# Optimization experiments

Hardware: AMD Instinct MI355X
Metric: run time of the kernel (lower is better)

The kernel has to match this reference:

```python
import jax, jax.numpy as jnp
import numpy as np
from jax import lax

HEADS = 8
LN_EPS = 1e-5


def setup_inputs() -> dict:
    key = jax.random.key(0)
    k = jax.random.split(key, 8)
    B, C, H, W, r = 4, 64, 64, 64, 4
    T = H * W
    x = jax.random.normal(k[0], (B, C, H, W), dtype=jnp.float32)
    conv_w = jax.random.normal(k[1], (C, C, r, r), dtype=jnp.float32) * 0.02  # OIHW
    conv_b = jnp.zeros((C,), dtype=jnp.float32)
    ln_g = jnp.ones((C,), dtype=jnp.float32)
    ln_b = jnp.zeros((C,), dtype=jnp.float32)
    Wqkv = jax.random.normal(k[2], (C, 3 * C), dtype=jnp.float32) * 0.02  # to_qvk (no bias)
    W0 = jax.random.normal(k[3], (C, C), dtype=jnp.float32) * 0.02  # output proj (no bias)
    E = jax.random.normal(k[4], (T, T // 4), dtype=jnp.float32)  # Linformer proj (randn in torch fwd)
    return {"x": x, "conv_w": conv_w, "conv_b": conv_b, "ln_g": ln_g,
            "ln_b": ln_b, "Wqkv": Wqkv, "W0": W0, "E": E}


def _layernorm2d(y, g, b):
    # LayerNorm over channel dim of NCHW (torch: permute to NHWC, LN last dim)
    yt = y.transpose(0, 2, 3, 1)  # b h w c
    mu = yt.mean(-1, keepdims=True)
    var = ((yt - mu) ** 2).mean(-1, keepdims=True)
    yt = (yt - mu) * lax.rsqrt(var + LN_EPS) * g + b
    return yt.transpose(0, 3, 1, 2)


def reference(x, conv_w, conv_b, ln_g, ln_b, Wqkv, W0, E):
    B, C, H, W = x.shape
    T = H * W
    dh = C // HEADS
    r = conv_w.shape[-1]

    # reducer: conv(stride=r) + LayerNorm2d. NOTE: faithful to the torch module,
    # this result is computed but NEVER used by the output (dead code in source).
    red = lax.conv_general_dilated(x, conv_w, (r, r), 'VALID',
                                   dimension_numbers=('NCHW', 'OIHW', 'NCHW'))
    red = red + conv_b[None, :, None, None]
    _red = _layernorm2d(red, ln_g, ln_b)  # unused, matches source

    # tokens from full-resolution x: b c h w -> b (h w) c
    xf = x.reshape(B, C, T).transpose(0, 2, 1)  # [B,T,C]
    qkv = xf @ Wqkv  # [B,T,3C]
    # rearrange 'b t (d k h)' with k=3, h=HEADS -> composite order (d, k, h)
    qkv = qkv.reshape(B, T, dh, 3, HEADS)
    q = qkv[:, :, :, 0, :].transpose(0, 3, 1, 2)  # [B,h,T,d]
    kk = qkv[:, :, :, 1, :].transpose(0, 3, 1, 2)
    v = qkv[:, :, :, 2, :].transpose(0, 3, 1, 2)

    # Linformer low-rank projection of V and K: [B,h,T,d] x [T,k] -> [B,h,k,d]
    v = jnp.einsum('bhjd,jk->bhkd', v, E)
    kk = jnp.einsum('bhjd,jk->bhkd', kk, E)

    scale = dh ** -0.5
    scores = jnp.einsum('bhid,bhjd->bhij', q, kk) * scale  # [B,h,T,k]
    attn = jax.nn.softmax(scores, axis=-1)
    out = jnp.einsum('bhij,bhjd->bhid', attn, v)  # [B,h,T,d]

    out = out.transpose(0, 2, 1, 3).reshape(B, T, C)  # b h i d -> b i (h d)
    out = out @ W0  # [B,T,C]
    return out.transpose(0, 2, 1).reshape(B, C, H, W)
```

## Files before the change

### kernel.cpp

```cpp
#include <hip/hip_runtime.h>

#define T_DIM 4096
#define KD    1024
#define SCALE2 (0.35355339059327373f * 1.4426950408889634f)
#define XS_PITCH 264
#define XP_PITCH 17
#define WK_PITCH 136
#define VC_H 648

extern "C" __device__ float __ocml_native_exp2_f32(float);

typedef __attribute__((ext_vector_type(8))) short bf16x8;
typedef __attribute__((ext_vector_type(4))) float f32x4;
typedef __attribute__((ext_vector_type(16))) float f32x16;

__device__ inline unsigned short f2bf(float f) {
  unsigned u = __float_as_uint(f);
  unsigned r = u + 0x7fffu + ((u >> 16) & 1u);
  return (unsigned short)(r >> 16);
}

__device__ inline unsigned cvt_pk_bf16(float a, float b) {
  unsigned ua = __float_as_uint(a); ua += 0x7fffu + ((ua >> 16) & 1u);
  unsigned ub = __float_as_uint(b); ub += 0x7fffu + ((ub >> 16) & 1u);
  return (ua >> 16) | (ub & 0xffff0000u);
}

__device__ inline bf16x8 mk8(unsigned a, unsigned b, unsigned c, unsigned d) {
  union { unsigned u[4]; bf16x8 v; } x;
  x.u[0] = a; x.u[1] = b; x.u[2] = c; x.u[3] = d; return x.v;
}

__global__ __launch_bounds__(512) void k_front(const float* __restrict__ x,
                                               const float* __restrict__ E,
                                               const float* __restrict__ Wqkv,
                                               uint2* __restrict__ Kg,
                                               unsigned short* __restrict__ Vg,
                                               float* __restrict__ Q) {
  __shared__ __attribute__((aligned(16))) float SMEM[8 * 64 * XP_PITCH];
  __shared__ __attribute__((aligned(16))) float Wkvs[64 * WK_PITCH];
  unsigned short* xs = (unsigned short*)SMEM;
  float* XPs = SMEM;

  const int bid = blockIdx.x;
  const int tid = threadIdx.x;

  if (bid < 256) {
    const int kb = (bid & 7) + 8 * (bid >> 5);
    const int b  = (bid >> 3) & 3;
    const int k0 = kb * 16;
    const int lane = tid & 63, w = tid >> 6;
    const int li = lane & 15, lg = lane >> 4;

#pragma unroll
    for (int i = 0; i < 16; ++i) {
      const int idx = tid + i * 512;
      const int c = idx >> 7, j = idx & 127;
      const int cg = j >> 3, d = j & 7;
      const int sel = (cg < 8) ? 1 : 2, h = cg & 7;
      Wkvs[c * WK_PITCH + j] = Wqkv[c * 192 + sel * 8 + h + d * 24];
    }

    f32x4 acc[4] = {};
    const int tl  = (tid & 127) * 2;
    const int chp = tid >> 7;
    const int tloc = w * 32 + lg * 8;

    for (int ct = 0; ct < 16; ++ct) {
      const float* xb = x + ((size_t)b * 64 + chp) * T_DIM + ct * 256 + tl;
#pragma unroll 4
      for (int it = 0; it < 16; ++it) {
        const int c = it * 4 + chp;
        float2 v = *(const float2*)(xb + (size_t)(it * 4) * T_DIM);
        *(unsigned*)(&xs[c * XS_PITCH + tl]) = cvt_pk_bf16(v.x, v.y);
      }
      __syncthreads();

      const int tb = ct * 256 + tloc;
      float bv[8];
#pragma unroll
      for (int j = 0; j < 8; ++j)
        bv[j] = E[(size_t)(tb + j) * KD + k0 + li];
      bf16x8 bq = mk8(cvt_pk_bf16(bv[0], bv[1]), cvt_pk_bf16(bv[2], bv[3]),
                      cvt_pk_bf16(bv[4], bv[5]), cvt_pk_bf16(bv[6], bv[7]));
#pragma unroll
      for (int mt = 0; mt < 4; ++mt) {
        bf16x8 af8 = *(const bf16x8*)(&xs[(mt * 16 + li) * XS_PITCH + tloc]);
        acc[mt] = __builtin_amdgcn_mfma_f32_16x16x32_bf16(af8, bq, acc[mt], 0, 0, 0);
      }
      __syncthreads();
    }

#pragma unroll
    for (int mt = 0; mt < 4; ++mt)
#pragma unroll
      for (int r = 0; r < 4; ++r)
        XPs[(w * 64 + mt * 16 + lg * 4 + r) * XP_PITCH + li] = acc[mt][r];
    __syncthreads();

#pragma unroll
    for (int i = 0; i < 2; ++i) {
      const int idx = tid + i * 512;
      const int c = idx >> 4, k = idx & 15;
      float s = 0.f;
#pragma unroll
      for (int wp = 0; wp < 8; ++wp) s += XPs[(wp * 64 + c) * XP_PITCH + k];
      XPs[c * XP_PITCH + k] = s;
    }
    __syncthreads();

    {
      const int k  = tid & 15;
      const int cg = (tid >> 4) & 15;
      const int dh = tid >> 8;
      float a4[4] = {0.f, 0.f, 0.f, 0.f};
#pragma unroll 8
      for (int c = 0; c < 64; ++c) {
        const float xv = XPs[c * XP_PITCH + k];
        const float4 wv = *(const float4*)(&Wkvs[c * WK_PITCH + cg * 8 + dh * 4]);
        a4[0] += xv * wv.x; a4[1] += xv * wv.y;
        a4[2] += xv * wv.z; a4[3] += xv * wv.w;
      }
      const int h = cg & 7, bh = b * 8 + h, kk2 = k0 + k;
      if (cg < 8) {
        Kg[(size_t)bh * 2048 + kk2 * 2 + dh] =
            make_uint2(cvt_pk_bf16(a4[0] * SCALE2, a4[1] * SCALE2),
                       cvt_pk_bf16(a4[2] * SCALE2, a4[3] * SCALE2));
      } else {
#pragma unroll
        for (int d = 0; d < 4; ++d)
          Vg[(size_t)(bh * 8 + dh * 4 + d) * KD + kk2] = f2bf(a4[d]);
      }
    }
  } else {
    const int idx = bid - 256;
    const int g  = idx & 7;
    const int tt = (idx >> 3) & 7;
    const int b  = idx >> 6;
    const int t  = tt * 512 + tid;
    const int col0 = g * 24;

    float acc[8];
#pragma unroll
    for (int j = 0; j < 8; ++j) acc[j] = 0.f;
    const float* xb = x + (size_t)b * 64 * T_DIM + t;
#pragma unroll 4
    for (int c = 0; c < 64; ++c) {
      float xv = xb[(size_t)c * T_DIM];
      const float* wr = Wqkv + c * 192 + col0;
#pragma unroll
      for (int h = 0; h < 8; ++h) acc[h] += xv * wr[h];
    }
#pragma unroll
    for (int h = 0; h < 8; ++h)
      Q[(((size_t)(b * 8 + h)) * 8 + g) * T_DIM + t] = acc[h];
  }
}

__global__ __launch_bounds__(512, 4) void k_attn(const float* __restrict__ Q,
                                                 const uint2* __restrict__ Kg,
                                                 const unsigned short* __restrict__ Vg,
                                                 const float* __restrict__ W0,
                                                 float* __restrict__ out) {
  __shared__ __attribute__((aligned(16))) unsigned short Kc[2][8 * 64 * 8];
  __shared__ __attribute__((aligned(16))) unsigned short Vc[2][8 * VC_H];
  __shared__ __attribute__((aligned(16))) float W0s[64 * 64];

  const int iy = blockIdx.x;
  const int b  = blockIdx.y;
  const int tid = threadIdx.x;
  const int w = tid >> 6;
  const int lane = tid & 63;
  const int icol = lane & 31, half = lane >> 5;
  const int i0 = iy * 32;
  const int bh = b * 8 + w;

#pragma unroll
  for (int i = 0; i < 8; ++i) W0s[tid + i * 512] = W0[tid + i * 512];

  {
    const int bu = tid >> 8, h = (tid >> 5) & 7, j2 = tid & 31;
    *(unsigned*)(&Vc[bu][h * VC_H + 8 * 72 + j2 * 2]) = 0x3F803F80u;
  }

  bf16x8 qf8 = {};
  if (lane < 32) {
    const float* qp = Q + (size_t)bh * 8 * T_DIM + i0 + icol;
    float q0 = qp[0],          q1 = qp[T_DIM],     q2 = qp[2 * T_DIM];
    float q3 = qp[3 * T_DIM],  q4 = qp[4 * T_DIM], q5 = qp[5 * T_DIM];
    float q6 = qp[6 * T_DIM],  q7 = qp[7 * T_DIM];
    qf8 = mk8(cvt_pk_bf16(q0, q1), cvt_pk_bf16(q2, q3),
              cvt_pk_bf16(q4, q5), cvt_pk_bf16(q6, q7));
  }

  const uint4* kg4    = (const uint4*)Kg + (size_t)b * 8192;
  const unsigned* vg2 = (const unsigned*)Vg + (size_t)b * 32768;

  {
    const int h = tid >> 6, j = tid & 63;
    *(uint4*)(&Kc[0][(h * 64 + j) * 8]) = kg4[h * 1024 + j];
#pragma unroll
    for (int i = 0; i < 4; ++i) {
      const int idx = tid + i * 512;
      const int hh = idx >> 8, d = (idx >> 5) & 7, j2 = idx & 31;
      *(unsigned*)(&Vc[0][hh * VC_H + d * 72 + j2 * 2]) = vg2[(hh * 8 + d) * 512 + j2];
    }
  }
  __syncthreads();

  f32x16 accO = {};
  int buf = 0;
  for (int jc = 0; jc < 16; ++jc) {
    uint4 kreg = {}; unsigned vreg[4] = {};
    if (jc < 15) {
      const int h = tid >> 6, j = tid & 63;
      kreg = kg4[h * 1024 + (jc + 1) * 64 + j];
#pragma unroll
      for (int i = 0; i < 4; ++i) {
        const int idx = tid + i * 512;
        const int hh = idx >> 8, d = (idx >> 5) & 7, j2 = idx & 31;
        vreg[i] = vg2[(hh * 8 + d) * 512 + (jc + 1) * 32 + j2];
      }
    }

#pragma unroll
    for (int sub = 0; sub < 2; ++sub) {
      const int jl = sub * 32;
      bf16x8 kf8 = {};
      if (lane < 32) kf8 = *(const bf16x8*)(&Kc[buf][(w * 64 + jl + lane) * 8]);
      f32x16 z = {};
      __builtin_amdgcn_s_setprio(1);
      f32x16 st = __builtin_amdgcn_mfma_f32_32x32x16_bf16(kf8, qf8, z, 0, 0, 0);
      __builtin_amdgcn_s_setprio(0);

      unsigned e0, e1, e2, e3, e4, e5, e6, e7;
      {
        float p0  = __ocml_native_exp2_f32(st[0]),  p1  = __ocml_native_exp2_f32(st[1]);
        float p2  = __ocml_native_exp2_f32(st[2]),  p3  = __ocml_native_exp2_f32(st[3]);
        float p4  = __ocml_native_exp2_f32(st[4]),  p5  = __ocml_native_exp2_f32(st[5]);
        float p6  = __ocml_native_exp2_f32(st[6]),  p7  = __ocml_native_exp2_f32(st[7]);
        float p8  = __ocml_native_exp2_f32(st[8]),  p9  = __ocml_native_exp2_f32(st[9]);
        float p10 = __ocml_native_exp2_f32(st[10]), p11 = __ocml_native_exp2_f32(st[11]);
        float p12 = __ocml_native_exp2_f32(st[12]), p13 = __ocml_native_exp2_f32(st[13]);
        float p14 = __ocml_native_exp2_f32(st[14]), p15 = __ocml_native_exp2_f32(st[15]);
        asm("v_cvt_pk_bf16_f32 %0, %1, %2" : "=v"(e0) : "v"(p0),  "v"(p1));
        asm("v_cvt_pk_bf16_f32 %0, %1, %2" : "=v"(e1) : "v"(p2),  "v"(p3));
        asm("v_cvt_pk_bf16_f32 %0, %1, %2" : "=v"(e2) : "v"(p4),  "v"(p5));
        asm("v_cvt_pk_bf16_f32 %0, %1, %2" : "=v"(e3) : "v"(p6),  "v"(p7));
        asm("v_cvt_pk_bf16_f32 %0, %1, %2" : "=v"(e4) : "v"(p8),  "v"(p9));
        asm("v_cvt_pk_bf16_f32 %0, %1, %2" : "=v"(e5) : "v"(p10), "v"(p11));
        asm("v_cvt_pk_bf16_f32 %0, %1, %2" : "=v"(e6) : "v"(p12), "v"(p13));
        asm("v_cvt_pk_bf16_f32 %0, %1, %2" : "=v"(e7) : "v"(p14), "v"(p15));
      }
      asm("v_permlane32_swap_b32 %0, %1" : "+v"(e0), "+v"(e2));
      asm("v_permlane32_swap_b32 %0, %1" : "+v"(e1), "+v"(e3));
      asm("v_permlane32_swap_b32 %0, %1" : "+v"(e4), "+v"(e6));
      asm("v_permlane32_swap_b32 %0, %1" : "+v"(e5), "+v"(e7));

      bf16x8 va0 = {}, va1 = {};
      if (icol < 9) {
        const unsigned short* vp = &Vc[buf][w * VC_H + icol * 72 + jl + half * 8];
        va0 = *(const bf16x8*)(vp);
        va1 = *(const bf16x8*)(vp + 16);
      }
      __builtin_amdgcn_s_setprio(1);
      accO = __builtin_amdgcn_mfma_f32_32x32x16_bf16(va0, mk8(e0, e1, e2, e3), accO, 0, 0, 0);
      accO = __builtin_amdgcn_mfma_f32_32x32x16_bf16(va1, mk8(e4, e5, e6, e7), accO, 0, 0, 0);
      __builtin_amdgcn_s_setprio(0);
    }

    if (jc < 15) {
      const int h = tid >> 6, j = tid & 63;
      *(uint4*)(&Kc[buf ^ 1][(h * 64 + j) * 8]) = kreg;
#pragma unroll
      for (int i = 0; i < 4; ++i) {
        const int idx = tid + i * 512;
        const int hh = idx >> 8, d = (idx >> 5) & 7, j2 = idx & 31;
        *(unsigned*)(&Vc[buf ^ 1][hh * VC_H + d * 72 + j2 * 2]) = vreg[i];
      }
    }
    __syncthreads();
    buf ^= 1;
  }

  float* Os = (float*)Kc;
  {
    float inv = 1.0f / __shfl(accO[4], icol);
    if (lane < 32 || half) {
      float4 o = make_float4(accO[0] * inv, accO[1] * inv,
                             accO[2] * inv, accO[3] * inv);
      *(float2*)(&Os[icol * 66 + w * 8 + half * 4])     = make_float2(o.x, o.y);
      *(float2*)(&Os[icol * 66 + w * 8 + half * 4 + 2]) = make_float2(o.z, o.w);
    }
  }
  __syncthreads();

  {
    const int tok = tid & 31, cq = tid >> 5;
    float o4[4] = {0.f, 0.f, 0.f, 0.f};
#pragma unroll 8
    for (int hd = 0; hd < 64; ++hd) {
      const float ov = Os[tok * 66 + hd];
      const float4 wv = *(const float4*)(&W0s[hd * 64 + cq * 4]);
      o4[0] += ov * wv.x; o4[1] += ov * wv.y;
      o4[2] += ov * wv.z; o4[3] += ov * wv.w;
    }
#pragma unroll
    for (int cc = 0; cc < 4; ++cc)
      out[((size_t)b * 64 + cq * 4 + cc) * T_DIM + i0 + tok] = o4[cc];
  }
}

extern "C" void kernel_launch(void* const* d_in, const int* in_sizes, int n_in,
                              void* d_out, int out_size, void* d_ws, size_t ws_size,
                              hipStream_t stream) {
  const float* x    = (const float*)d_in[0];
  const float* Wqkv = (const float*)d_in[5];
  const float* W0   = (const float*)d_in[6];
  const float* E    = (const float*)d_in[7];
  float* out = (float*)d_out;

  float* Q           = (float*)d_ws;
  uint2* Kg          = (uint2*)(Q + 1048576);
  unsigned short* Vg = (unsigned short*)(Kg + 65536);

  k_front <<<dim3(512),    512, 0, stream>>>(x, E, Wqkv, Kg, Vg, Q);
  k_attn  <<<dim3(128, 4), 512, 0, stream>>>(Q, Kg, Vg, W0, out);
}
```

Measured before the change: 139.8 us.

## Double-buffer x tiles and prefetch E into registers in front kernel

The x·E projection loop in the front kernel now software-pipelines its work. Global loads of the next x tile and E fragment are issued into registers before the current tile's MFMAs run, then converted and written into an alternate LDS buffer, so only one barrier per iteration remains. The Wqkv staging into LDS moves after the loop, with Wkvs and XPs aliased into a single shared array to make room for the second buffer. This hides global-load latency behind compute, at the cost of higher register pressure from holding 16 float2 plus 8 floats in flight.

```diff
diff --git a/kernel.cpp b/kernel.cpp
--- a/kernel.cpp
+++ b/kernel.cpp
@@ -37,10 +37,11 @@
                                                uint2* __restrict__ Kg,
                                                unsigned short* __restrict__ Vg,
                                                float* __restrict__ Q) {
-  __shared__ __attribute__((aligned(16))) float SMEM[8 * 64 * XP_PITCH];
-  __shared__ __attribute__((aligned(16))) float Wkvs[64 * WK_PITCH];
-  unsigned short* xs = (unsigned short*)SMEM;
-  float* XPs = SMEM;
+  __shared__ __attribute__((aligned(16))) float SMEM[17408];
+  unsigned short* xs0 = (unsigned short*)SMEM;
+  unsigned short* xs1 = xs0 + 64 * XS_PITCH;
+  float* XPs  = SMEM;
+  float* Wkvs = SMEM + 8704;
 
   const int bid = blockIdx.x;
   const int tid = threadIdx.x;
@@ -52,6 +53,66 @@
     const int lane = tid & 63, w = tid >> 6;
     const int li = lane & 15, lg = lane >> 4;
 
+    const int tl  = (tid & 127) * 2;
+    const int chp = tid >> 7;
+    const int tloc = w * 32 + lg * 8;
+
+    bf16x8 bq;
+    {
+      const float* xb = x + ((size_t)b * 64 + chp) * T_DIM + tl;
+      float2 xr[16];
+#pragma unroll
+      for (int it = 0; it < 16; ++it)
+        xr[it] = *(const float2*)(xb + (size_t)(it * 4) * T_DIM);
+      float ev[8];
+#pragma unroll
+      for (int j = 0; j < 8; ++j)
+        ev[j] = E[(size_t)(tloc + j) * KD + k0 + li];
+#pragma unroll
+      for (int it = 0; it < 16; ++it)
+        *(unsigned*)(&xs0[(it * 4 + chp) * XS_PITCH + tl]) = cvt_pk_bf16(xr[it].x, xr[it].y);
+      bq = mk8(cvt_pk_bf16(ev[0], ev[1]), cvt_pk_bf16(ev[2], ev[3]),
+               cvt_pk_bf16(ev[4], ev[5]), cvt_pk_bf16(ev[6], ev[7]));
+    }
+    __syncthreads();
+
+    f32x4 acc[4] = {};
+    for (int ct = 0; ct < 16; ++ct) {
+      unsigned short* rb = (ct & 1) ? xs1 : xs0;
+      unsigned short* wb = (ct & 1) ? xs0 : xs1;
+
+      float2 xr[16]; float evn[8];
+      if (ct < 15) {
+        const float* xb = x + ((size_t)b * 64 + chp) * T_DIM + (ct + 1) * 256 + tl;
+#pragma unroll
+        for (int it = 0; it < 16; ++it)
+          xr[it] = *(const float2*)(xb + (size_t)(it * 4) * T_DIM);
+#pragma unroll
+        for (int j = 0; j < 8; ++j)
+          evn[j] = E[(size_t)((ct + 1) * 256 + tloc + j) * KD + k0 + li];
+      }
+
+#pragma unroll
+      for (int mt = 0; mt < 4; ++mt) {
+        bf16x8 af8 = *(const bf16x8*)(&rb[(mt * 16 + li) * XS_PITCH + tloc]);
+        acc[mt] = __builtin_amdgcn_mfma_f32_16x16x32_bf16(af8, bq, acc[mt], 0, 0, 0);
+      }
+
+      if (ct < 15) {
+#pragma unroll
+        for (int it = 0; it < 16; ++it)
+          *(unsigned*)(&wb[(it * 4 + chp) * XS_PITCH + tl]) = cvt_pk_bf16(xr[it].x, xr[it].y);
+        bq = mk8(cvt_pk_bf16(evn[0], evn[1]), cvt_pk_bf16(evn[2], evn[3]),
+                 cvt_pk_bf16(evn[4], evn[5]), cvt_pk_bf16(evn[6], evn[7]));
+      }
+      __syncthreads();
+    }
+
+#pragma unroll
+    for (int mt = 0; mt < 4; ++mt)
+#pragma unroll
+      for (int r = 0; r < 4; ++r)
+        XPs[(w * 64 + mt * 16 + lg * 4 + r) * XP_PITCH + li] = acc[mt][r];
 #pragma unroll
     for (int i = 0; i < 16; ++i) {
       const int idx = tid + i * 512;
@@ -60,42 +121,6 @@
       const int sel = (cg < 8) ? 1 : 2, h = cg & 7;
       Wkvs[c * WK_PITCH + j] = Wqkv[c * 192 + sel * 8 + h + d * 24];
     }
-
-    f32x4 acc[4] = {};
-    const int tl  = (tid & 127) * 2;
-    const int chp = tid >> 7;
-    const int tloc = w * 32 + lg * 8;
-
-    for (int ct = 0; ct < 16; ++ct) {
-      const float* xb = x + ((size_t)b * 64 + chp) * T_DIM + ct * 256 + tl;
-#pragma unroll 4
-      for (int it = 0; it < 16; ++it) {
-        const int c = it * 4 + chp;
-        float2 v = *(const float2*)(xb + (size_t)(it * 4) * T_DIM);
-        *(unsigned*)(&xs[c * XS_PITCH + tl]) = cvt_pk_bf16(v.x, v.y);
-      }
-      __syncthreads();
-
-      const int tb = ct * 256 + tloc;
-      float bv[8];
-#pragma unroll
-      for (int j = 0; j < 8; ++j)
-        bv[j] = E[(size_t)(tb + j) * KD + k0 + li];
-      bf16x8 bq = mk8(cvt_pk_bf16(bv[0], bv[1]), cvt_pk_bf16(bv[2], bv[3]),
-                      cvt_pk_bf16(bv[4], bv[5]), cvt_pk_bf16(bv[6], bv[7]));
-#pragma unroll
-      for (int mt = 0; mt < 4; ++mt) {
-        bf16x8 af8 = *(const bf16x8*)(&xs[(mt * 16 + li) * XS_PITCH + tloc]);
-        acc[mt] = __builtin_amdgcn_mfma_f32_16x16x32_bf16(af8, bq, acc[mt], 0, 0, 0);
-      }
-      __syncthreads();
-    }
-
-#pragma unroll
-    for (int mt = 0; mt < 4; ++mt)
-#pragma unroll
-      for (int r = 0; r < 4; ++r)
-        XPs[(w * 64 + mt * 16 + lg * 4 + r) * XP_PITCH + li] = acc[mt][r];
     __syncthreads();
 
 #pragma unroll
```

Measured after the change: 135.7 us. 2.9% less time.

## Widen front kernel blocks to 1024 threads covering 32 Linformer columns each

Applied to the files above, without the earlier changes.

Rebuilds the K/V Linformer projection in k_front so each block has 1024 threads and computes 32 k-columns instead of 16. Each block loads 512-token tiles of x once and reuses them for two MFMA accumulator sets, which halves the redundant x reads across blocks. E loads are now issued before the x staging to overlap latency, and the Q blocks are resized to 1024 threads. This uses more LDS and more registers per block and halves the block count, which may lower occupancy.

```diff
diff --git a/kernel.cpp b/kernel.cpp
--- a/kernel.cpp
+++ b/kernel.cpp
@@ -3,7 +3,7 @@
 #define T_DIM 4096
 #define KD    1024
 #define SCALE2 (0.35355339059327373f * 1.4426950408889634f)
-#define XS_PITCH 264
+#define XS2_PITCH 520
 #define XP_PITCH 17
 #define WK_PITCH 136
 #define VC_H 648
@@ -31,92 +31,99 @@
   x.u[0] = a; x.u[1] = b; x.u[2] = c; x.u[3] = d; return x.v;
 }
 
-__global__ __launch_bounds__(512) void k_front(const float* __restrict__ x,
-                                               const float* __restrict__ E,
-                                               const float* __restrict__ Wqkv,
-                                               uint2* __restrict__ Kg,
-                                               unsigned short* __restrict__ Vg,
-                                               float* __restrict__ Q) {
-  __shared__ __attribute__((aligned(16))) float SMEM[8 * 64 * XP_PITCH];
+__global__ __launch_bounds__(1024) void k_front(const float* __restrict__ x,
+                                                const float* __restrict__ E,
+                                                const float* __restrict__ Wqkv,
+                                                uint2* __restrict__ Kg,
+                                                unsigned short* __restrict__ Vg,
+                                                float* __restrict__ Q) {
+  __shared__ __attribute__((aligned(16))) float SMEM[17408];
   __shared__ __attribute__((aligned(16))) float Wkvs[64 * WK_PITCH];
+  __shared__ __attribute__((aligned(16))) float XPfull[64 * 33];
   unsigned short* xs = (unsigned short*)SMEM;
   float* XPs = SMEM;
 
   const int bid = blockIdx.x;
   const int tid = threadIdx.x;
 
-  if (bid < 256) {
-    const int kb = (bid & 7) + 8 * (bid >> 5);
-    const int b  = (bid >> 3) & 3;
-    const int k0 = kb * 16;
+  if (bid < 128) {
+    const int kb2 = (bid & 7) + 8 * (bid >> 5);
+    const int b   = (bid >> 3) & 3;
+    const int k0  = kb2 * 32;
     const int lane = tid & 63, w = tid >> 6;
     const int li = lane & 15, lg = lane >> 4;
 
 #pragma unroll
-    for (int i = 0; i < 16; ++i) {
-      const int idx = tid + i * 512;
+    for (int i = 0; i < 8; ++i) {
+      const int idx = tid + i * 1024;
       const int c = idx >> 7, j = idx & 127;
       const int cg = j >> 3, d = j & 7;
       const int sel = (cg < 8) ? 1 : 2, h = cg & 7;
       Wkvs[c * WK_PITCH + j] = Wqkv[c * 192 + sel * 8 + h + d * 24];
     }
 
-    f32x4 acc[4] = {};
-    const int tl  = (tid & 127) * 2;
-    const int chp = tid >> 7;
+    const int tl  = (tid & 255) * 2;
+    const int chp = tid >> 8;
     const int tloc = w * 32 + lg * 8;
 
-    for (int ct = 0; ct < 16; ++ct) {
-      const float* xb = x + ((size_t)b * 64 + chp) * T_DIM + ct * 256 + tl;
+    f32x4 acc[4][2] = {};
+    for (int ct = 0; ct < 8; ++ct) {
+      float ev0[8], ev1[8];
+      const int tb = ct * 512 + tloc;
+#pragma unroll
+      for (int j = 0; j < 8; ++j) {
+        ev0[j] = E[(size_t)(tb + j) * KD + k0 + li];
+        ev1[j] = E[(size_t)(tb + j) * KD + k0 + 16 + li];
+      }
+
+      const float* xb = x + ((size_t)b * 64 + chp) * T_DIM + ct * 512 + tl;
 #pragma unroll 4
       for (int it = 0; it < 16; ++it) {
         const int c = it * 4 + chp;
         float2 v = *(const float2*)(xb + (size_t)(it * 4) * T_DIM);
-        *(unsigned*)(&xs[c * XS_PITCH + tl]) = cvt_pk_bf16(v.x, v.y);
+        *(unsigned*)(&xs[c * XS2_PITCH + tl]) = cvt_pk_bf16(v.x, v.y);
       }
       __syncthreads();
 
-      const int tb = ct * 256 + tloc;
-      float bv[8];
-#pragma unroll
-      for (int j = 0; j < 8; ++j)
-        bv[j] = E[(size_t)(tb + j) * KD + k0 + li];
-      bf16x8 bq = mk8(cvt_pk_bf16(bv[0], bv[1]), cvt_pk_bf16(bv[2], bv[3]),
-                      cvt_pk_bf16(bv[4], bv[5]), cvt_pk_bf16(bv[6], bv[7]));
+      bf16x8 bq0 = mk8(cvt_pk_bf16(ev0[0], ev0[1]), cvt_pk_bf16(ev0[2], ev0[3]),
+                       cvt_pk_bf16(ev0[4], ev0[5]), cvt_pk_bf16(ev0[6], ev0[7]));
+      bf16x8 bq1 = mk8(cvt_pk_bf16(ev1[0], ev1[1]), cvt_pk_bf16(ev1[2], ev1[3]),
+                       cvt_pk_bf16(ev1[4], ev1[5]), cvt_pk_bf16(ev1[6], ev1[7]));
 #pragma unroll
       for (int mt = 0; mt < 4; ++mt) {
-        bf16x8 af8 = *(const bf16x8*)(&xs[(mt * 16 + li) * XS_PITCH + tloc]);
-        acc[mt] = __builtin_amdgcn_mfma_f32_16x16x32_bf16(af8, bq, acc[mt], 0, 0, 0);
+        bf16x8 af8 = *(const bf16x8*)(&xs[(mt * 16 + li) * XS2_PITCH + tloc]);
+        acc[mt][0] = __builtin_amdgcn_mfma_f32_16x16x32_bf16(af8, bq0, acc[mt][0], 0, 0, 0);
+        acc[mt][1] = __builtin_amdgcn_mfma_f32_16x16x32_bf16(af8, bq1, acc[mt][1], 0, 0, 0);
       }
       __syncthreads();
     }
 
 #pragma unroll
-    for (int mt = 0; mt < 4; ++mt)
-#pragma unroll
-      for (int r = 0; r < 4; ++r)
-        XPs[(w * 64 + mt * 16 + lg * 4 + r) * XP_PITCH + li] = acc[mt][r];
-    __syncthreads();
-
-#pragma unroll
-    for (int i = 0; i < 2; ++i) {
-      const int idx = tid + i * 512;
-      const int c = idx >> 4, k = idx & 15;
-      float s = 0.f;
-#pragma unroll
-      for (int wp = 0; wp < 8; ++wp) s += XPs[(wp * 64 + c) * XP_PITCH + k];
-      XPs[c * XP_PITCH + k] = s;
-    }
-    __syncthreads();
+    for (int g = 0; g < 2; ++g) {
+#pragma unroll
+      for (int mt = 0; mt < 4; ++mt)
+#pragma unroll
+        for (int r = 0; r < 4; ++r)
+          XPs[(w * 64 + mt * 16 + lg * 4 + r) * XP_PITCH + li] = acc[mt][g][r];
+      __syncthreads();
+      {
+        const int c = tid >> 4, k = tid & 15;
+        float s = 0.f;
+#pragma unroll
+        for (int wp = 0; wp < 16; ++wp) s += XPs[(wp * 64 + c) * XP_PITCH + k];
+        XPfull[c * 33 + g * 16 + k] = s;
+      }
+      __syncthreads();
+    }
 
     {
-      const int k  = tid & 15;
-      const int cg = (tid >> 4) & 15;
-      const int dh = tid >> 8;
+      const int k  = tid & 31;
+      const int cg = (tid >> 5) & 15;
+      const int dh = tid >> 9;
       float a4[4] = {0.f, 0.f, 0.f, 0.f};
 #pragma unroll 8
       for (int c = 0; c < 64; ++c) {
-        const float xv = XPs[c * XP_PITCH + k];
+        const float xv = XPfull[c * 33 + k];
         const float4 wv = *(const float4*)(&Wkvs[c * WK_PITCH + cg * 8 + dh * 4]);
         a4[0] += xv * wv.x; a4[1] += xv * wv.y;
         a4[2] += xv * wv.z; a4[3] += xv * wv.w;
@@ -133,11 +140,11 @@
       }
     }
   } else {
-    const int idx = bid - 256;
+    const int idx = bid - 128;
     const int g  = idx & 7;
-    const int tt = (idx >> 3) & 7;
-    const int b  = idx >> 6;
-    const int t  = tt * 512 + tid;
+    const int tt = (idx >> 3) & 3;
+    const int b  = idx >> 5;
+    const int t  = tt * 1024 + tid;
     const int col0 = g * 24;
 
     float acc[8];
@@ -324,6 +331,6 @@
   uint2* Kg          = (uint2*)(Q + 1048576);
   unsigned short* Vg = (unsigned short*)(Kg + 65536);
 
-  k_front <<<dim3(512),    512, 0, stream>>>(x, E, Wqkv, Kg, Vg, Q);
-  k_attn  <<<dim3(128, 4), 512, 0, stream>>>(Q, Kg, Vg, W0, out);
-}
+  k_front <<<dim3(256),    1024, 0, stream>>>(x, E, Wqkv, Kg, Vg, Q);
+  k_attn  <<<dim3(128, 4), 512,  0, stream>>>(Q, Kg, Vg, W0, out);
+}
```

Result: no change. 137.1 us (-1.9%).
